# Optimization experiments

Hardware: AMD Instinct MI355X
Metric: run time of the kernel (lower is better)

The kernel has to match this reference:

```python
import jax, jax.numpy as jnp
import numpy as np

IN_C, DIM, OUT_C, N_PIECES = 3, 256, 256, 20
BATCH, SET_N = 16, 128


def _xavier(k, shape, fan_in, fan_out):
    limit = float(np.sqrt(6.0 / (fan_in + fan_out)))
    return jax.random.uniform(k, shape, jnp.float32, -limit, limit)


def setup_inputs() -> dict:
    key = jax.random.key(0)
    ks = jax.random.split(key, 9)
    return {
        "x": jax.random.normal(ks[0], (BATCH, IN_C, SET_N), jnp.float32),
        "conv1_w": _xavier(ks[1], (DIM, IN_C), IN_C, DIM),
        "conv1_b": jnp.zeros((DIM,), jnp.float32),
        "conv2_w": _xavier(ks[2], (DIM, DIM), DIM, DIM),
        "conv2_b": jnp.zeros((DIM,), jnp.float32),
        "pool_w": jax.random.normal(ks[3], (DIM, N_PIECES + 1), jnp.float32) * 0.1,
        "lin1_w": _xavier(ks[4], (DIM, DIM), DIM, DIM),
        "lin1_b": jnp.zeros((DIM,), jnp.float32),
        "lin2_w": _xavier(ks[5], (OUT_C, DIM), DIM, OUT_C),
        "lin2_b": jnp.zeros((OUT_C,), jnp.float32),
        "cls1_w": _xavier(ks[6], (OUT_C, OUT_C), OUT_C, OUT_C),
        "cls1_b": jnp.zeros((OUT_C,), jnp.float32),
        "cls2_w": _xavier(ks[7], (10, OUT_C), OUT_C, 10),
        "cls2_b": jnp.zeros((10,), jnp.float32),
    }


def _fspool(x, pool_w, tau=1.0):
    # x: (B, C, N); pool_w: (C, N_PIECES+1). n is None -> full sets, mask is all ones.
    B, C, N = x.shape
    # piecewise-linear continuous weights evaluated at ratios i/(N-1)
    ratios = jnp.clip(jnp.arange(N, dtype=x.dtype) / max(N - 1, 1), 0.0, 1.0)  # (N,)
    idx_f = N_PIECES * ratios
    idx = jnp.floor(idx_f).astype(jnp.int32)
    frac = idx_f - idx.astype(x.dtype)
    left = pool_w[:, idx]                                   # (C, N)
    right = pool_w[:, jnp.clip(idx + 1, 0, N_PIECES)]       # (C, N)
    w = (1.0 - frac) * left + frac * right                  # (C, N)
    # relaxed continuous sort (NeuralSort / deterministic_sort), descending
    s = x.reshape(B * C, N, 1)
    A = jnp.abs(s - jnp.swapaxes(s, 1, 2))                  # (BC, N, N)
    Bsum = A.sum(axis=2, keepdims=True)                     # == A @ 1 1^T rowsums, (BC, N, 1)
    scaling = (N + 1 - 2 * (jnp.arange(N) + 1)).astype(x.dtype)  # (N,)
    Cmat = s * scaling[None, None, :]                       # (BC, N, N)
    P = jax.nn.softmax(jnp.swapaxes(Cmat - Bsum, 1, 2) / tau, axis=-1)  # (BC, N, N)
    xs = jnp.matmul(P, s).reshape(B, C, N)                  # soft-sorted, descending
    pooled = (xs * w[None]).sum(axis=2)                     # (B, C)
    return pooled, P


def reference(x, conv1_w, conv1_b, conv2_w, conv2_b, pool_w,
              lin1_w, lin1_b, lin2_w, lin2_b, cls1_w, cls1_b, cls2_w, cls2_b):
    # conv1x1 stack: (B, IN_C, N) -> (B, DIM, N)
    h = jnp.einsum('dc,bcn->bdn', conv1_w, x) + conv1_b[None, :, None]
    h = jax.nn.relu(h)
    h = jnp.einsum('dc,bcn->bdn', conv2_w, h) + conv2_b[None, :, None]
    pooled, _ = _fspool(h, pool_w)                          # (B, DIM)
    z = jax.nn.relu(pooled @ lin1_w.T + lin1_b)
    z = z @ lin2_w.T + lin2_b                               # (B, OUT_C)
    z = jax.nn.relu(z @ cls1_w.T + cls1_b)
    return z @ cls2_w.T + cls2_b                            # (B, 10)
```

## Files before the change

kernel.cpp:

```cpp
#include <hip/hip_runtime.h>
#include <math.h>


#if __has_builtin(__builtin_amdgcn_exp2f)
#define EXP2F(x) __builtin_amdgcn_exp2f(x)
#else
#define EXP2F(x) exp2f(x)
#endif

__device__ __forceinline__ float pool_weight(const float* __restrict__ pw, int j)
{
    float ratio = (float)j / 127.0f;
    float idx_f = 20.0f * ratio;
    int idx = (int)idx_f;
    float frac = idx_f - (float)idx;
    int idx2 = idx + 1 > 20 ? 20 : idx + 1;
    return (1.0f - frac) * pw[idx] + frac * pw[idx2];
}

__global__ __launch_bounds__(256, 8) void conv_pool_kernel(
    const float* __restrict__ x,   const float* __restrict__ w1,
    const float* __restrict__ b1,  const float* __restrict__ W2,
    const float* __restrict__ b2,  const float* __restrict__ pool_w,
    float* __restrict__ pooled)
{
    const float LOG2E = 1.4426950408889634f;
    __shared__ __align__(16) float4 w1p[256];
    __shared__ __align__(16) float  Ast[2][16];
    __shared__ __align__(16) float2 Bsp[16][66];
    __shared__ __align__(16) float  ss[2][128];
    __shared__ __align__(16) float  bb[2][128];
    __shared__ float partial[4];

    int tid = threadIdx.x;
    int blk = blockIdx.x;
    int b   = blk >> 7;
    int c0  = (blk & 127) << 1;

    int wid = tid >> 6, l = tid & 63;
    int r   = wid & 1,  h = wid >> 1;
    int ng  = tid & 31, kg = tid >> 5;
    int n0  = ng * 2;

    w1p[tid] = make_float4(w1[tid*3], w1[tid*3+1], w1[tid*3+2], b1[tid]);
    const float* xb = x + b * 384;
    float x00 = xb[n0],            x01 = xb[n0 + 1];
    float x0a = xb[n0 + 64],       x0b = xb[n0 + 65];
    float x10 = xb[128 + n0],      x11 = xb[128 + n0 + 1];
    float x1a = xb[128 + n0 + 64], x1b = xb[128 + n0 + 65];
    float x20 = xb[256 + n0],      x21 = xb[256 + n0 + 1];
    float x2a = xb[256 + n0 + 64], x2b = xb[256 + n0 + 65];
    __syncthreads();

    float acc0 = 0.f, acc1 = 0.f;

    for (int k0 = 0; k0 < 256; k0 += 16) {
        if (tid < 32)
            Ast[tid >> 4][tid & 15] =
                W2[(c0 + (tid >> 4)) * 256 + k0 + (tid & 15)];
        #pragma unroll
        for (int q = 0; q < 2; q++) {
            int krel = kg * 2 + q;
            float4 wv = w1p[k0 + krel];
            float h0 = fmaxf(fmaf(wv.x,x00, fmaf(wv.y,x10, fmaf(wv.z,x20, wv.w))), 0.f);
            float h1 = fmaxf(fmaf(wv.x,x01, fmaf(wv.y,x11, fmaf(wv.z,x21, wv.w))), 0.f);
            float ha = fmaxf(fmaf(wv.x,x0a, fmaf(wv.y,x1a, fmaf(wv.z,x2a, wv.w))), 0.f);
            float hb = fmaxf(fmaf(wv.x,x0b, fmaf(wv.y,x1b, fmaf(wv.z,x2b, wv.w))), 0.f);
            *(float4*)&Bsp[krel][n0] = make_float4(h0, ha, h1, hb);
        }
        __syncthreads();
        if (wid < 2) {
            float4 a4[4];
            #pragma unroll
            for (int q = 0; q < 4; q++)
                a4[q] = *(const float4*)&Ast[wid][q * 4];
            #pragma unroll
            for (int kk = 0; kk < 16; kk++) {
                float a = ((const float*)a4)[kk];
                float2 bv = Bsp[kk][l];
                acc0 = fmaf(a, bv.x, acc0);
                acc1 = fmaf(a, bv.y, acc1);
            }
        }
        __syncthreads();
    }

    if (wid < 2) {
        float bias = b2[c0 + wid];
        ss[wid][l]      = acc0 + bias;
        ss[wid][l + 64] = acc1 + bias;
    }
    __syncthreads();

    int i = h * 64 + l;
    float si = ss[r][i];

    float a0 = 0.f, a1 = 0.f, a2 = 0.f, a3 = 0.f;
    #pragma unroll 8
    for (int j = 0; j < 128; j += 4) {
        float4 s4 = *(const float4*)&ss[r][j];
        a0 += fabsf(si - s4.x); a1 += fabsf(si - s4.y);
        a2 += fabsf(si - s4.z); a3 += fabsf(si - s4.w);
    }
    bb[r][i] = ((a0 + a1) + (a2 + a3)) * LOG2E;
    __syncthreads();

    float scal = (float)(127 - 2 * i) * LOG2E;
    float m0 = -1e30f, m1 = -1e30f, m2 = -1e30f, m3 = -1e30f;
    #pragma unroll 8
    for (int k = 0; k < 128; k += 4) {
        float4 s4 = *(const float4*)&ss[r][k];
        float4 b4 = *(const float4*)&bb[r][k];
        m0 = fmaxf(m0, fmaf(s4.x, scal, -b4.x));
        m1 = fmaxf(m1, fmaf(s4.y, scal, -b4.y));
        m2 = fmaxf(m2, fmaf(s4.z, scal, -b4.z));
        m3 = fmaxf(m3, fmaf(s4.w, scal, -b4.w));
    }
    float m = fmaxf(fmaxf(m0, m1), fmaxf(m2, m3));

    float se0 = 0.f, se1 = 0.f, se2 = 0.f, se3 = 0.f;
    float sd0 = 0.f, sd1 = 0.f, sd2 = 0.f, sd3 = 0.f;
    #pragma unroll 4
    for (int k = 0; k < 128; k += 4) {
        float4 s4 = *(const float4*)&ss[r][k];
        float4 b4 = *(const float4*)&bb[r][k];
        float e0 = EXP2F(fmaf(s4.x, scal, -b4.x) - m);
        float e1 = EXP2F(fmaf(s4.y, scal, -b4.y) - m);
        float e2 = EXP2F(fmaf(s4.z, scal, -b4.z) - m);
        float e3 = EXP2F(fmaf(s4.w, scal, -b4.w) - m);
        se0 += e0; sd0 = fmaf(e0, s4.x, sd0);
        se1 += e1; sd1 = fmaf(e1, s4.y, sd1);
        se2 += e2; sd2 = fmaf(e2, s4.z, sd2);
        se3 += e3; sd3 = fmaf(e3, s4.w, sd3);
    }
    float xs = ((sd0 + sd1) + (sd2 + sd3)) / ((se0 + se1) + (se2 + se3));

    float part = xs * pool_weight(pool_w + (c0 + r) * 21, i);
    #pragma unroll
    for (int off = 32; off > 0; off >>= 1)
        part += __shfl_xor(part, off);
    if (l == 0) partial[wid] = part;
    __syncthreads();
    if (tid < 2)
        pooled[b * 256 + c0 + tid] = partial[tid] + partial[tid + 2];
}

__device__ __forceinline__ void dense512(
    const float* __restrict__ W, const float* __restrict__ Bv,
    const float* in_lds, float* out_lds, int tid, bool do_relu)
{
    int o = tid >> 1, p = tid & 1;
    const float* wr = W + o * 256 + p * 128;
    const float* ir = in_lds + p * 128;
    float acc = 0.f;
    #pragma unroll
    for (int k = 0; k < 128; k += 4) {
        float4 wv = *(const float4*)(wr + k);
        float4 iv = *(const float4*)(ir + k);
        acc = fmaf(wv.x, iv.x, acc); acc = fmaf(wv.y, iv.y, acc);
        acc = fmaf(wv.z, iv.z, acc); acc = fmaf(wv.w, iv.w, acc);
    }
    acc += __shfl_xor(acc, 1);
    if (p == 0) {
        acc += Bv[o];
        out_lds[o] = do_relu ? fmaxf(acc, 0.f) : acc;
    }
}

__global__ __launch_bounds__(512) void tail_kernel(
    const float* __restrict__ pooled,
    const float* __restrict__ L1w, const float* __restrict__ L1b,
    const float* __restrict__ L2w, const float* __restrict__ L2b,
    const float* __restrict__ C1w, const float* __restrict__ C1b,
    const float* __restrict__ C2w, const float* __restrict__ C2b,
    float* __restrict__ out)
{
    __shared__ float za[256], zb[256];
    int bt = blockIdx.x, tid = threadIdx.x;
    if (tid < 256) za[tid] = pooled[bt * 256 + tid];
    __syncthreads();
    dense512(L1w, L1b, za, zb, tid, true);
    __syncthreads();
    dense512(L2w, L2b, zb, za, tid, false);
    __syncthreads();
    dense512(C1w, C1b, za, zb, tid, true);
    __syncthreads();
    if (tid < 320) {
        int o = tid >> 5, kb = tid & 31;
        const float* wr = C2w + o * 256 + kb * 8;
        const float* ir = zb + kb * 8;
        float4 w0 = *(const float4*)(wr);
        float4 w1v = *(const float4*)(wr + 4);
        float4 i0 = *(const float4*)(ir);
        float4 i1 = *(const float4*)(ir + 4);
        float p = fmaf(w0.x,i0.x, fmaf(w0.y,i0.y, fmaf(w0.z,i0.z,
                  fmaf(w0.w,i0.w, fmaf(w1v.x,i1.x, fmaf(w1v.y,i1.y,
                  fmaf(w1v.z,i1.z, w1v.w*i1.w)))))));
        #pragma unroll
        for (int off = 16; off > 0; off >>= 1)
            p += __shfl_xor(p, off, 32);
        if (kb == 0) out[bt * 10 + o] = p + C2b[o];
    }
}

extern "C" void kernel_launch(void* const* d_in, const int* in_sizes, int n_in,
                              void* d_out, int out_size, void* d_ws, size_t ws_size,
                              hipStream_t stream)
{
    (void)in_sizes; (void)n_in; (void)out_size; (void)ws_size;
    const float* x       = (const float*)d_in[0];
    const float* conv1_w = (const float*)d_in[1];
    const float* conv1_b = (const float*)d_in[2];
    const float* conv2_w = (const float*)d_in[3];
    const float* conv2_b = (const float*)d_in[4];
    const float* pool_w  = (const float*)d_in[5];
    const float* lin1_w  = (const float*)d_in[6];
    const float* lin1_b  = (const float*)d_in[7];
    const float* lin2_w  = (const float*)d_in[8];
    const float* lin2_b  = (const float*)d_in[9];
    const float* cls1_w  = (const float*)d_in[10];
    const float* cls1_b  = (const float*)d_in[11];
    const float* cls2_w  = (const float*)d_in[12];
    const float* cls2_b  = (const float*)d_in[13];
    float* out = (float*)d_out;

    float* pooled = (float*)d_ws;

    conv_pool_kernel<<<2048, 256, 0, stream>>>(
        x, conv1_w, conv1_b, conv2_w, conv2_b, pool_w, pooled);
    tail_kernel<<<16, 512, 0, stream>>>(pooled,
        lin1_w, lin1_b, lin2_w, lin2_b, cls1_w, cls1_b, cls2_w, cls2_b, out);
}
```

Baseline: 65.57 us.

## Process four channels per block with split-K conv2 across all threads

```diff
diff --git a/kernel.cpp b/kernel.cpp
--- a/kernel.cpp
+++ b/kernel.cpp
@@ -7,6 +7,8 @@
 #else
 #define EXP2F(x) exp2f(x)
 #endif
+
+#define LOG2E 1.4426950408889634f
 
 __device__ __forceinline__ float pool_weight(const float* __restrict__ pw, int j)
 {
@@ -18,95 +20,104 @@
     return (1.0f - frac) * pw[idx] + frac * pw[idx2];
 }
 
-__global__ __launch_bounds__(256, 8) void conv_pool_kernel(
+__global__ __launch_bounds__(512, 8) void conv_pool_kernel(
     const float* __restrict__ x,   const float* __restrict__ w1,
     const float* __restrict__ b1,  const float* __restrict__ W2,
     const float* __restrict__ b2,  const float* __restrict__ pool_w,
     float* __restrict__ pooled)
 {
-    const float LOG2E = 1.4426950408889634f;
-    __shared__ __align__(16) float4 w1p[256];
-    __shared__ __align__(16) float  Ast[2][16];
-    __shared__ __align__(16) float2 Bsp[16][66];
-    __shared__ __align__(16) float  ss[2][128];
-    __shared__ __align__(16) float  bb[2][128];
-    __shared__ float partial[4];
+    __shared__ float4 w1p[256];
+    __shared__ float4 AstT[32];
+    __shared__ float2 Bsp2[16][132];
+    __shared__ float4 Part[4][128];
+    __shared__ float  ss[4][128];
+    __shared__ float  bb[4][128];
+    __shared__ float  partial[8];
 
     int tid = threadIdx.x;
     int blk = blockIdx.x;
-    int b   = blk >> 7;
-    int c0  = (blk & 127) << 1;
-
+    int b   = blk >> 6;
+    int c0  = (blk & 63) << 2;
+
+    int k2 = tid >> 5;
+    int n0 = (tid & 31) * 4;
+    int col = tid & 127;
+    int kq  = tid >> 7;
     int wid = tid >> 6, l = tid & 63;
-    int r   = wid & 1,  h = wid >> 1;
-    int ng  = tid & 31, kg = tid >> 5;
-    int n0  = ng * 2;
-
-    w1p[tid] = make_float4(w1[tid*3], w1[tid*3+1], w1[tid*3+2], b1[tid]);
+    int r   = wid & 3,  h = wid >> 2;
+    int i   = h * 64 + l;
+
+    if (tid < 256)
+        w1p[tid] = make_float4(w1[tid*3], w1[tid*3+1], w1[tid*3+2], b1[tid]);
     const float* xb = x + b * 384;
-    float x00 = xb[n0],            x01 = xb[n0 + 1];
-    float x0a = xb[n0 + 64],       x0b = xb[n0 + 65];
-    float x10 = xb[128 + n0],      x11 = xb[128 + n0 + 1];
-    float x1a = xb[128 + n0 + 64], x1b = xb[128 + n0 + 65];
-    float x20 = xb[256 + n0],      x21 = xb[256 + n0 + 1];
-    float x2a = xb[256 + n0 + 64], x2b = xb[256 + n0 + 65];
-    __syncthreads();
-
-    float acc0 = 0.f, acc1 = 0.f;
-
-    for (int k0 = 0; k0 < 256; k0 += 16) {
-        if (tid < 32)
-            Ast[tid >> 4][tid & 15] =
-                W2[(c0 + (tid >> 4)) * 256 + k0 + (tid & 15)];
-        #pragma unroll
-        for (int q = 0; q < 2; q++) {
-            int krel = kg * 2 + q;
-            float4 wv = w1p[k0 + krel];
-            float h0 = fmaxf(fmaf(wv.x,x00, fmaf(wv.y,x10, fmaf(wv.z,x20, wv.w))), 0.f);
-            float h1 = fmaxf(fmaf(wv.x,x01, fmaf(wv.y,x11, fmaf(wv.z,x21, wv.w))), 0.f);
-            float ha = fmaxf(fmaf(wv.x,x0a, fmaf(wv.y,x1a, fmaf(wv.z,x2a, wv.w))), 0.f);
-            float hb = fmaxf(fmaf(wv.x,x0b, fmaf(wv.y,x1b, fmaf(wv.z,x2b, wv.w))), 0.f);
-            *(float4*)&Bsp[krel][n0] = make_float4(h0, ha, h1, hb);
+    float4 xc0 = *(const float4*)(xb + n0);
+    float4 xc1 = *(const float4*)(xb + 128 + n0);
+    float4 xc2 = *(const float4*)(xb + 256 + n0);
+    __syncthreads();
+
+    float ac0 = 0.f, ac1 = 0.f, ac2 = 0.f, ac3 = 0.f;
+
+    for (int k0 = 0; k0 < 256; k0 += 32) {
+        if (tid < 32) {
+            int k = k0 + tid;
+            AstT[tid] = make_float4(W2[(c0+0)*256 + k], W2[(c0+1)*256 + k],
+                                    W2[(c0+2)*256 + k], W2[(c0+3)*256 + k]);
+        }
+        {
+            float4 wv0 = w1p[k0 + 2*k2];
+            float4 wv1 = w1p[k0 + 2*k2 + 1];
+            float h00 = fmaxf(fmaf(wv0.x,xc0.x, fmaf(wv0.y,xc1.x, fmaf(wv0.z,xc2.x, wv0.w))), 0.f);
+            float h01 = fmaxf(fmaf(wv0.x,xc0.y, fmaf(wv0.y,xc1.y, fmaf(wv0.z,xc2.y, wv0.w))), 0.f);
+            float h02 = fmaxf(fmaf(wv0.x,xc0.z, fmaf(wv0.y,xc1.z, fmaf(wv0.z,xc2.z, wv0.w))), 0.f);
+            float h03 = fmaxf(fmaf(wv0.x,xc0.w, fmaf(wv0.y,xc1.w, fmaf(wv0.z,xc2.w, wv0.w))), 0.f);
+            float h10 = fmaxf(fmaf(wv1.x,xc0.x, fmaf(wv1.y,xc1.x, fmaf(wv1.z,xc2.x, wv1.w))), 0.f);
+            float h11 = fmaxf(fmaf(wv1.x,xc0.y, fmaf(wv1.y,xc1.y, fmaf(wv1.z,xc2.y, wv1.w))), 0.f);
+            float h12 = fmaxf(fmaf(wv1.x,xc0.z, fmaf(wv1.y,xc1.z, fmaf(wv1.z,xc2.z, wv1.w))), 0.f);
+            float h13 = fmaxf(fmaf(wv1.x,xc0.w, fmaf(wv1.y,xc1.w, fmaf(wv1.z,xc2.w, wv1.w))), 0.f);
+            *(float4*)&Bsp2[k2][n0]     = make_float4(h00, h10, h01, h11);
+            *(float4*)&Bsp2[k2][n0 + 2] = make_float4(h02, h12, h03, h13);
         }
         __syncthreads();
-        if (wid < 2) {
-            float4 a4[4];
-            #pragma unroll
-            for (int q = 0; q < 4; q++)
-                a4[q] = *(const float4*)&Ast[wid][q * 4];
-            #pragma unroll
-            for (int kk = 0; kk < 16; kk++) {
-                float a = ((const float*)a4)[kk];
-                float2 bv = Bsp[kk][l];
-                acc0 = fmaf(a, bv.x, acc0);
-                acc1 = fmaf(a, bv.y, acc1);
-            }
+        #pragma unroll
+        for (int p = 0; p < 4; p++) {
+            int t = 4*p + kq;
+            float2 bv = Bsp2[t][col];
+            float4 a0 = AstT[2*t];
+            float4 a1 = AstT[2*t + 1];
+            ac0 = fmaf(a0.x, bv.x, ac0); ac0 = fmaf(a1.x, bv.y, ac0);
+            ac1 = fmaf(a0.y, bv.x, ac1); ac1 = fmaf(a1.y, bv.y, ac1);
+            ac2 = fmaf(a0.z, bv.x, ac2); ac2 = fmaf(a1.z, bv.y, ac2);
+            ac3 = fmaf(a0.w, bv.x, ac3); ac3 = fmaf(a1.w, bv.y, ac3);
         }
         __syncthreads();
     }
 
-    if (wid < 2) {
-        float bias = b2[c0 + wid];
-        ss[wid][l]      = acc0 + bias;
-        ss[wid][l + 64] = acc1 + bias;
-    }
-    __syncthreads();
-
-    int i = h * 64 + l;
-    float si = ss[r][i];
-
-    float a0 = 0.f, a1 = 0.f, a2 = 0.f, a3 = 0.f;
+    Part[kq][col] = make_float4(ac0, ac1, ac2, ac3);
+    __syncthreads();
+    const float* pf = (const float*)Part;
+    float s_own;
+    {
+        float v0 = pf[(0*128 + i)*4 + r];
+        float v1 = pf[(1*128 + i)*4 + r];
+        float v2 = pf[(2*128 + i)*4 + r];
+        float v3 = pf[(3*128 + i)*4 + r];
+        s_own = ((v0 + v1) + (v2 + v3)) + b2[c0 + r];
+        ss[r][i] = s_own;
+    }
+    __syncthreads();
+
+    float sa0=0.f, sa1=0.f, sa2=0.f, sa3=0.f;
     #pragma unroll 8
     for (int j = 0; j < 128; j += 4) {
         float4 s4 = *(const float4*)&ss[r][j];
-        a0 += fabsf(si - s4.x); a1 += fabsf(si - s4.y);
-        a2 += fabsf(si - s4.z); a3 += fabsf(si - s4.w);
-    }
-    bb[r][i] = ((a0 + a1) + (a2 + a3)) * LOG2E;
-    __syncthreads();
-
-    float scal = (float)(127 - 2 * i) * LOG2E;
-    float m0 = -1e30f, m1 = -1e30f, m2 = -1e30f, m3 = -1e30f;
+        sa0 += fabsf(s_own - s4.x); sa1 += fabsf(s_own - s4.y);
+        sa2 += fabsf(s_own - s4.z); sa3 += fabsf(s_own - s4.w);
+    }
+    bb[r][i] = ((sa0+sa1)+(sa2+sa3)) * LOG2E;
+    __syncthreads();
+
+    float scal = (float)(127 - 2*i) * LOG2E;
+    float m0=-1e30f, m1=-1e30f, m2=-1e30f, m3=-1e30f;
     #pragma unroll 8
     for (int k = 0; k < 128; k += 4) {
         float4 s4 = *(const float4*)&ss[r][k];
@@ -118,8 +129,8 @@
     }
     float m = fmaxf(fmaxf(m0, m1), fmaxf(m2, m3));
 
-    float se0 = 0.f, se1 = 0.f, se2 = 0.f, se3 = 0.f;
-    float sd0 = 0.f, sd1 = 0.f, sd2 = 0.f, sd3 = 0.f;
+    float se0=0.f, se1=0.f, se2=0.f, se3=0.f;
+    float sd0=0.f, sd1=0.f, sd2=0.f, sd3=0.f;
     #pragma unroll 4
     for (int k = 0; k < 128; k += 4) {
         float4 s4 = *(const float4*)&ss[r][k];
@@ -133,7 +144,7 @@
         se2 += e2; sd2 = fmaf(e2, s4.z, sd2);
         se3 += e3; sd3 = fmaf(e3, s4.w, sd3);
     }
-    float xs = ((sd0 + sd1) + (sd2 + sd3)) / ((se0 + se1) + (se2 + se3));
+    float xs = ((sd0+sd1)+(sd2+sd3)) / ((se0+se1)+(se2+se3));
 
     float part = xs * pool_weight(pool_w + (c0 + r) * 21, i);
     #pragma unroll
@@ -141,8 +152,8 @@
         part += __shfl_xor(part, off);
     if (l == 0) partial[wid] = part;
     __syncthreads();
-    if (tid < 2)
-        pooled[b * 256 + c0 + tid] = partial[tid] + partial[tid + 2];
+    if (tid < 4)
+        pooled[b * 256 + c0 + tid] = partial[tid] + partial[tid + 4];
 }
 
 __device__ __forceinline__ void dense512(
@@ -226,7 +237,7 @@
 
     float* pooled = (float*)d_ws;
 
-    conv_pool_kernel<<<2048, 256, 0, stream>>>(
+    conv_pool_kernel<<<1024, 512, 0, stream>>>(
         x, conv1_w, conv1_b, conv2_w, conv2_b, pool_w, pooled);
     tail_kernel<<<16, 512, 0, stream>>>(pooled,
         lin1_w, lin1_b, lin2_w, lin2_b, cls1_w, cls1_b, cls2_w, cls2_b, out);
```

Measured after the change: 57.49 us. 1.14x faster.
